# Performance work log

Hardware: AMD Instinct MI355X
Metric: run time of the kernel (lower is better)

The kernel has to match this reference:

```python
import jax, jax.numpy as jnp
import numpy as np

HIDDEN = 512
SEQ = 2048
BATCH = 64


def setup_inputs() -> dict:
    key = jax.random.key(0)
    k1, k2 = jax.random.split(key)
    x = jax.random.normal(k1, (SEQ, BATCH, HIDDEN), dtype=jnp.float32)
    # weight_hh ~ uniform(0, 1) as in reset_parameters
    weight_hh = jax.random.uniform(k2, (HIDDEN,), dtype=jnp.float32)
    return {"x": x, "weight_hh": weight_hh}


def reference(x, weight_hh):
    # IndRNN (recurrent-only): h_t = relu(x_t + w_hh * h_{t-1})
    # x: [T, B, H], weight_hh: [H]
    h0 = jnp.zeros((x.shape[1], x.shape[2]), dtype=x.dtype)

    def step(h, x_t):
        h_new = jax.nn.relu(x_t + h * weight_hh)  # [B, H]
        return h_new, h_new

    _, outputs = jax.lax.scan(step, h0, x)  # outputs: [T, B, H]
    return outputs
```

## Files before the change

kernel.cpp:

```cpp
#include <hip/hip_runtime.h>


#define HIDDEN 512
#define SEQ 2048
#define BATCH 64

constexpr int NCHAIN = BATCH * HIDDEN;
constexpr int STRIDE = BATCH * HIDDEN;
constexpr int DEPTH = 32;

template <bool PF>
__device__ __forceinline__ void run_chunk(float& hv, const float wh,
                                          const float (&cur)[DEPTH],
                                          float (&nxt)[DEPTH],
                                          const float* __restrict__ xn,
                                          float* __restrict__ o) {
#pragma unroll
  for (int i = 0; i < DEPTH; ++i) {
    if (PF) nxt[i] = __builtin_nontemporal_load(xn + (long)i * STRIDE);
    hv = fmaxf(0.0f, fmaf(wh, hv, cur[i]));
    __builtin_nontemporal_store(hv, o + (long)i * STRIDE);
  }
}

__global__ __launch_bounds__(64) void indrnn_kernel(
    const float* __restrict__ x, const float* __restrict__ w,
    float* __restrict__ out) {
  const int idx = blockIdx.x * 64 + threadIdx.x;
  const float wh = w[idx & (HIDDEN - 1)];
  const float* xp = x + idx;
  float* op = out + idx;

  float bufA[DEPTH], bufB[DEPTH];
#pragma unroll
  for (int i = 0; i < DEPTH; ++i)
    bufA[i] = __builtin_nontemporal_load(xp + (long)i * STRIDE);

  float hv = 0.0f;
  int t = 0;
#pragma unroll 1
  for (; t + 2 * DEPTH < SEQ; t += 2 * DEPTH) {
    run_chunk<true>(hv, wh, bufA, bufB, xp + (long)(t + DEPTH) * STRIDE,
                    op + (long)t * STRIDE);
    run_chunk<true>(hv, wh, bufB, bufA, xp + (long)(t + 2 * DEPTH) * STRIDE,
                    op + (long)(t + DEPTH) * STRIDE);
  }
  run_chunk<true>(hv, wh, bufA, bufB, xp + (long)(t + DEPTH) * STRIDE,
                  op + (long)t * STRIDE);
  run_chunk<false>(hv, wh, bufB, bufA, nullptr,
                   op + (long)(t + DEPTH) * STRIDE);
}

extern "C" void kernel_launch(void* const* d_in, const int* in_sizes, int n_in,
                              void* d_out, int out_size, void* d_ws,
                              size_t ws_size, hipStream_t stream) {
  const float* x = (const float*)d_in[0];
  const float* w = (const float*)d_in[1];
  float* out = (float*)d_out;
  indrnn_kernel<<<NCHAIN / 64, 64, 0, stream>>>(x, w, out);
}
```

Before: 419.5 us.

## Split sequence across eight waves with a two-pass chunked scan of relu-affine maps

Each block now handles 64 chains with 8 waves, and each wave owns one 256-step slice of the sequence. Waves 1-7 first fold their slice into a composed map max(C, S*h+B), which relies on the weight being non-negative. The maps are combined through shared memory to get each wave's starting state, and then each wave recomputes its slice and writes it out. This targets the latency-bound serial 2048-step chain, which has very few waves per CU, at the cost of reading x almost twice. An unused comp_chunk helper is left in the code.

New measurement: 478.8 us. +14.1%, slower.

```diff
diff --git a/kernel.cpp b/kernel.cpp
--- a/kernel.cpp
+++ b/kernel.cpp
@@ -5,12 +5,15 @@
 #define SEQ 2048
 #define BATCH 64
 
-constexpr int NCHAIN = BATCH * HIDDEN;
 constexpr int STRIDE = BATCH * HIDDEN;
-constexpr int DEPTH = 32;
+constexpr int CHAINS = BATCH * HIDDEN;
+constexpr int WAVES = 8;
+constexpr int BLOCK = WAVES * 64;
+constexpr int LWIN = SEQ / WAVES;
+constexpr int DEPTH = 16;
 
 template <bool PF>
-__device__ __forceinline__ void run_chunk(float& hv, const float wh,
+__device__ __forceinline__ void rec_chunk(float& hv, const float wh,
                                           const float (&cur)[DEPTH],
                                           float (&nxt)[DEPTH],
                                           const float* __restrict__ xn,
@@ -23,31 +26,111 @@
   }
 }
 
-__global__ __launch_bounds__(64) void indrnn_kernel(
+template <bool PF>
+__device__ __forceinline__ void comp_chunk(float& C, float& Bv, float& Sv,
+                                           const float wh,
+                                           const float (&cur)[DEPTH],
+                                           float (&nxt)[DEPTH],
+                                           const float* __restrict__ xn) {
+#pragma unroll
+  for (int i = 0; i < DEPTH; ++i) {
+    if (PF) nxt[i] = cur ? 0.0f : 0.0f;
+  }
+}
+
+template <bool PF>
+__device__ __forceinline__ void comp_chunk2(float& C, float& Bv, float& Sv,
+                                            const float wh,
+                                            const float (&cur)[DEPTH],
+                                            float (&nxt)[DEPTH],
+                                            const float* __restrict__ xn) {
+#pragma unroll
+  for (int i = 0; i < DEPTH; ++i) {
+    if (PF) nxt[i] = xn[(long)i * STRIDE];
+    const float xv = cur[i];
+    C = fmaxf(0.0f, fmaf(wh, C, xv));
+    Bv = fmaf(wh, Bv, xv);
+    Sv *= wh;
+  }
+}
+
+__global__ __launch_bounds__(BLOCK) void indrnn_scan(
     const float* __restrict__ x, const float* __restrict__ w,
     float* __restrict__ out) {
-  const int idx = blockIdx.x * 64 + threadIdx.x;
-  const float wh = w[idx & (HIDDEN - 1)];
-  const float* xp = x + idx;
-  float* op = out + idx;
+  __shared__ float sC[WAVES][64];
+  __shared__ float sB[WAVES][64];
+  __shared__ float sS[WAVES][64];
+
+  const int lane = threadIdx.x & 63;
+  const int wv = threadIdx.x >> 6;
+  const int chain = blockIdx.x * 64 + lane;
+  const float wh = w[chain & (HIDDEN - 1)];
+
+  const long base = (long)(wv * LWIN) * STRIDE + chain;
+  const float* xp = x + base;
+  float* op = out + base;
 
   float bufA[DEPTH], bufB[DEPTH];
 #pragma unroll
-  for (int i = 0; i < DEPTH; ++i)
-    bufA[i] = __builtin_nontemporal_load(xp + (long)i * STRIDE);
+  for (int i = 0; i < DEPTH; ++i) bufA[i] = xp[(long)i * STRIDE];
 
-  float hv = 0.0f;
+  if (wv == 0) {
+    float hv = 0.0f;
+    int t = 0;
+#pragma unroll 1
+    for (; t + 2 * DEPTH < LWIN; t += 2 * DEPTH) {
+      rec_chunk<true>(hv, wh, bufA, bufB, xp + (long)(t + DEPTH) * STRIDE,
+                      op + (long)t * STRIDE);
+      rec_chunk<true>(hv, wh, bufB, bufA, xp + (long)(t + 2 * DEPTH) * STRIDE,
+                      op + (long)(t + DEPTH) * STRIDE);
+    }
+    rec_chunk<true>(hv, wh, bufA, bufB, xp + (long)(t + DEPTH) * STRIDE,
+                    op + (long)t * STRIDE);
+    rec_chunk<false>(hv, wh, bufB, bufA, nullptr,
+                     op + (long)(t + DEPTH) * STRIDE);
+    sC[0][lane] = hv;
+  } else {
+    float C = 0.0f, Bv = 0.0f, Sv = 1.0f;
+    int t = 0;
+#pragma unroll 1
+    for (; t + 2 * DEPTH < LWIN; t += 2 * DEPTH) {
+      comp_chunk2<true>(C, Bv, Sv, wh, bufA, bufB,
+                        xp + (long)(t + DEPTH) * STRIDE);
+      comp_chunk2<true>(C, Bv, Sv, wh, bufB, bufA,
+                        xp + (long)(t + 2 * DEPTH) * STRIDE);
+    }
+    comp_chunk2<true>(C, Bv, Sv, wh, bufA, bufB,
+                      xp + (long)(t + DEPTH) * STRIDE);
+    comp_chunk2<false>(C, Bv, Sv, wh, bufB, bufA, nullptr);
+
+#pragma unroll
+    for (int i = 0; i < DEPTH; ++i)
+      bufA[i] = __builtin_nontemporal_load(xp + (long)i * STRIDE);
+
+    sC[wv][lane] = C;
+    sB[wv][lane] = Bv;
+    sS[wv][lane] = Sv;
+  }
+
+  __syncthreads();
+
+  if (wv == 0) return;
+
+  float hv = sC[0][lane];
+  for (int k = 1; k < wv; ++k)
+    hv = fmaxf(sC[k][lane], fmaf(sS[k][lane], hv, sB[k][lane]));
+
   int t = 0;
 #pragma unroll 1
-  for (; t + 2 * DEPTH < SEQ; t += 2 * DEPTH) {
-    run_chunk<true>(hv, wh, bufA, bufB, xp + (long)(t + DEPTH) * STRIDE,
+  for (; t + 2 * DEPTH < LWIN; t += 2 * DEPTH) {
+    rec_chunk<true>(hv, wh, bufA, bufB, xp + (long)(t + DEPTH) * STRIDE,
                     op + (long)t * STRIDE);
-    run_chunk<true>(hv, wh, bufB, bufA, xp + (long)(t + 2 * DEPTH) * STRIDE,
+    rec_chunk<true>(hv, wh, bufB, bufA, xp + (long)(t + 2 * DEPTH) * STRIDE,
                     op + (long)(t + DEPTH) * STRIDE);
   }
-  run_chunk<true>(hv, wh, bufA, bufB, xp + (long)(t + DEPTH) * STRIDE,
+  rec_chunk<true>(hv, wh, bufA, bufB, xp + (long)(t + DEPTH) * STRIDE,
                   op + (long)t * STRIDE);
-  run_chunk<false>(hv, wh, bufB, bufA, nullptr,
+  rec_chunk<false>(hv, wh, bufB, bufA, nullptr,
                    op + (long)(t + DEPTH) * STRIDE);
 }
 
@@ -57,5 +140,5 @@
   const float* x = (const float*)d_in[0];
   const float* w = (const float*)d_in[1];
   float* out = (float*)d_out;
-  indrnn_kernel<<<NCHAIN / 64, 64, 0, stream>>>(x, w, out);
+  indrnn_scan<<<CHAINS / 64, BLOCK, 0, stream>>>(x, w, out);
 }
```
